# Optimization experiments

Measured on AMD Instinct MI355X. Metric: run time of the kernel, lower is better.

The kernel has to match this reference:

```python
import jax, jax.numpy as jnp
import numpy as np

B, S, E = 2, 2048, 2048
NQ, NKV, HD = 16, 4, 128
WINDOW = 512
ROPE_BASE = 10000.0


def _rope(x):
    # x: [B, H, S, HD], interleaved even/odd rotation
    half = HD // 2
    freqs = 1.0 / (ROPE_BASE ** (2.0 * jnp.arange(half, dtype=jnp.float32) / HD))
    pos = jnp.arange(x.shape[2], dtype=jnp.float32)
    ang = pos[:, None] * freqs[None, :]            # [S, HD/2]
    cos = jnp.cos(ang)[None, None].astype(x.dtype)  # [1,1,S,HD/2]
    sin = jnp.sin(ang)[None, None].astype(x.dtype)
    xe = x[..., 0::2]
    xo = x[..., 1::2]
    re = xe * cos - xo * sin
    ro = xe * sin + xo * cos
    return jnp.stack([re, ro], axis=-1).reshape(x.shape)


def setup_inputs() -> dict:
    key = jax.random.key(0)
    ks = jax.random.split(key, 9)
    s_in = 1.0 / np.sqrt(E)
    s_out = 1.0 / np.sqrt(NQ * HD)
    return {
        "x": jax.random.normal(ks[0], (B, S, E), jnp.float32),
        "Wq": jax.random.normal(ks[1], (E, NQ * HD), jnp.float32) * s_in,
        "bq": jax.random.normal(ks[2], (NQ * HD,), jnp.float32) * 0.01,
        "Wk": jax.random.normal(ks[3], (E, NKV * HD), jnp.float32) * s_in,
        "bk": jax.random.normal(ks[4], (NKV * HD,), jnp.float32) * 0.01,
        "Wv": jax.random.normal(ks[5], (E, NKV * HD), jnp.float32) * s_in,
        "bv": jax.random.normal(ks[6], (NKV * HD,), jnp.float32) * 0.01,
        "Wo": jax.random.normal(ks[7], (NQ * HD, E), jnp.float32) * s_out,
        "bo": jax.random.normal(ks[8], (E,), jnp.float32) * 0.01,
    }


def reference(x, Wq, bq, Wk, bk, Wv, bv, Wo, bo):
    b, s, _ = x.shape
    q = (x @ Wq + bq).reshape(b, s, NQ, HD).transpose(0, 2, 1, 3)   # [B,NQ,S,HD]
    k = (x @ Wk + bk).reshape(b, s, NKV, HD).transpose(0, 2, 1, 3)  # [B,NKV,S,HD]
    v = (x @ Wv + bv).reshape(b, s, NKV, HD).transpose(0, 2, 1, 3)
    q = _rope(q)
    k = _rope(k)
    rep = NQ // NKV
    k = jnp.repeat(k, rep, axis=1)  # [B,NQ,S,HD], matches torch repeat pattern
    v = jnp.repeat(v, rep, axis=1)
    scores = jnp.einsum("bhqd,bhkd->bhqk", q, k) / np.sqrt(HD)
    i = jnp.arange(s)[:, None]
    j = jnp.arange(s)[None, :]
    allowed = (j <= i) & ((i - j) <= WINDOW)  # sliding-window causal mask
    scores = jnp.where(allowed[None, None], scores, -jnp.inf)
    weights = jax.nn.softmax(scores, axis=-1)
    out = jnp.einsum("bhqk,bhkd->bhqd", weights, v)
    out = out.transpose(0, 2, 1, 3).reshape(b, s, NQ * HD)
    return out @ Wo + bo
```

## Files before the change

kernel.cpp:

```cpp
#include <hip/hip_runtime.h>
#include <hip/hip_bf16.h>
#include <math.h>

#define BB 2
#define SS 2048
#define EE 2048
#define NQ 16
#define NKV 4
#define HD 128
#define WINDOW 512

typedef __hip_bfloat16 bf16;
typedef short short8 __attribute__((ext_vector_type(8)));
typedef float f32x4 __attribute__((ext_vector_type(4)));

__device__ __forceinline__ float toF(bf16 v) { return __bfloat162float(v); }
__device__ __forceinline__ bf16 toB(float v) { return __float2bfloat16(v); }

__device__ __forceinline__ void gld_lds16(const void* g, void* l) {
    __builtin_amdgcn_global_load_lds(
        (const __attribute__((address_space(1))) void*)g,
        (__attribute__((address_space(3))) void*)l, 16, 0, 0);
}

__global__ __launch_bounds__(256) void convert_bf16(const float* __restrict__ in,
                                                    bf16* __restrict__ out, int n) {
    int i = (blockIdx.x * 256 + threadIdx.x) * 4;
    if (i >= n) return;
    const float4 v = *(const float4*)(in + i);
    bf16 o[4] = {toB(v.x), toB(v.y), toB(v.z), toB(v.w)};
    *(uint2*)(out + i) = *(const uint2*)o;
}

__global__ __launch_bounds__(256) void convert_transpose(const float* __restrict__ in,
                                                         bf16* __restrict__ out,
                                                         int K, int N) {
    __shared__ float tile[32][33];
    const int t = threadIdx.x;
    const int tx = t & 31, ty = t >> 5;
    const int n0 = blockIdx.x * 32, k0 = blockIdx.y * 32;
#pragma unroll
    for (int r = 0; r < 4; r++) {
        int k = k0 + ty + r * 8;
        tile[ty + r * 8][tx] = in[(size_t)k * N + n0 + tx];
    }
    __syncthreads();
#pragma unroll
    for (int r = 0; r < 4; r++) {
        int n = n0 + ty + r * 8;
        out[(size_t)n * K + k0 + tx] = toB(tile[tx][ty + r * 8]);
    }
}

template <int MODE>
__global__ __launch_bounds__(256) void mfma_gemm(
    const bf16* __restrict__ A, const bf16* __restrict__ BT,
    const float* __restrict__ b0, const float* __restrict__ b1,
    const float* __restrict__ b2,
    float* __restrict__ Yf,
    bf16* __restrict__ Yq, bf16* __restrict__ Yk, bf16* __restrict__ Yv,
    int M, int N, int K) {
    __shared__ bf16 As[128 * 32];
    __shared__ bf16 Bs[128 * 32];

    const int t = threadIdx.x;
    const int lane = t & 63;
    const int w = t >> 6;
    const int wm = w >> 1, wn = w & 1;
    const int m0 = blockIdx.y * 128, n0 = blockIdx.x * 128;

    const int srow = lane >> 2;
    const int scol = (lane & 3) * 8;

    f32x4 acc[4][4];
#pragma unroll
    for (int i = 0; i < 4; i++)
#pragma unroll
        for (int j = 0; j < 4; j++) acc[i][j] = (f32x4)0.f;

    const int lr = lane & 15;
    const int lq = lane >> 4;

    for (int k0 = 0; k0 < K; k0 += 32) {
#pragma unroll
        for (int s = 0; s < 2; s++) {
            const int c = w * 2 + s;
            gld_lds16(A + (size_t)(m0 + c * 16 + srow) * K + k0 + scol, As + c * 512);
            gld_lds16(BT + (size_t)(n0 + c * 16 + srow) * K + k0 + scol, Bs + c * 512);
        }
        __syncthreads();
        short8 af[4], bfv[4];
#pragma unroll
        for (int i = 0; i < 4; i++)
            af[i] = *(const short8*)(As + (wm * 64 + i * 16 + lr) * 32 + lq * 8);
#pragma unroll
        for (int j = 0; j < 4; j++)
            bfv[j] = *(const short8*)(Bs + (wn * 64 + j * 16 + lr) * 32 + lq * 8);
#pragma unroll
        for (int i = 0; i < 4; i++)
#pragma unroll
            for (int j = 0; j < 4; j++)
                acc[i][j] = __builtin_amdgcn_mfma_f32_16x16x32_bf16(af[i], bfv[j],
                                                                    acc[i][j], 0, 0, 0);
        __syncthreads();
    }

    if (MODE == 0) {
#pragma unroll
        for (int j = 0; j < 4; j++) {
            const int col = n0 + wn * 64 + j * 16 + lr;
            const float bj = b0[col];
#pragma unroll
            for (int i = 0; i < 4; i++) {
                const int row = m0 + wm * 64 + i * 16 + lq * 4;
#pragma unroll
                for (int r = 0; r < 4; r++)
                    Yf[(size_t)(row + r) * N + col] = acc[i][j][r] + bj;
            }
        }
    } else {
        bf16* outp; const float* bias; int ldc, c0;
        if (n0 < 2048)      { outp = Yq; bias = b0; ldc = 2048; c0 = n0; }
        else if (n0 < 2560) { outp = Yk; bias = b1; ldc = 512;  c0 = n0 - 2048; }
        else                { outp = Yv; bias = b2; ldc = 512;  c0 = n0 - 2560; }
#pragma unroll
        for (int j = 0; j < 4; j++) {
            const int col = c0 + wn * 64 + j * 16 + lr;
            const float bj = bias[col];
#pragma unroll
            for (int i = 0; i < 4; i++) {
                const int row = m0 + wm * 64 + i * 16 + lq * 4;
#pragma unroll
                for (int r = 0; r < 4; r++)
                    outp[(size_t)(row + r) * ldc + col] = toB(acc[i][j][r] + bj);
            }
        }
    }
}

__global__ void rope_kernel(bf16* __restrict__ buf, int H) {
    int idx = blockIdx.x * blockDim.x + threadIdx.x;
    int total = BB * SS * H * (HD / 2);
    if (idx >= total) return;
    int d2 = idx & 63;
    int hh = idx >> 6;
    int h = hh % H;
    int row = hh / H;
    int s = row % SS;
    float freq = expf(-logf(10000.f) * (float)(2 * d2) / (float)HD);
    float ang = (float)s * freq;
    float c = cosf(ang), sn = sinf(ang);
    size_t base = ((size_t)row * H + h) * HD + 2 * d2;
    float xe = toF(buf[base]);
    float xo = toF(buf[base + 1]);
    buf[base]     = toB(xe * c - xo * sn);
    buf[base + 1] = toB(xe * sn + xo * c);
}

__global__ __launch_bounds__(256) void attn_mfma(const bf16* __restrict__ Q,
                                                 const bf16* __restrict__ K,
                                                 const bf16* __restrict__ V,
                                                 bf16* __restrict__ Oout) {
    __shared__ bf16 Ks[64 * 128];
    __shared__ bf16 Vt[128 * 72];
    __shared__ bf16 Ps[4 * 16 * 72];

    const int t = threadIdx.x;
    const int lane = t & 63;
    const int w = t >> 6;
    const int q0 = blockIdx.x * 64;
    const int h = blockIdx.y;
    const int b = blockIdx.z;
    const int hkv = h >> 2;
    const int lr = lane & 15;
    const int lq = lane >> 4;
    const float scale = 0.08838834764831845f;

    short8 aq[4];
    {
        const int q = q0 + w * 16 + lr;
        const bf16* qp = Q + (((size_t)b * SS + q) * NQ + h) * HD + lq * 8;
#pragma unroll
        for (int ks = 0; ks < 4; ks++) aq[ks] = *(const short8*)(qp + ks * 32);
    }

    f32x4 Oa[8];
#pragma unroll
    for (int nb = 0; nb < 8; nb++) Oa[nb] = (f32x4)0.f;
    float mprev[4] = {-3.0e38f, -3.0e38f, -3.0e38f, -3.0e38f};
    float lsum[4] = {0.f, 0.f, 0.f, 0.f};

    bf16* Pw = Ps + w * 16 * 72;
    const int jstart = (q0 >= WINDOW) ? (q0 - WINDOW) : 0;

    for (int c0 = jstart; c0 <= q0; c0 += 64) {
        __syncthreads();
#pragma unroll
        for (int s = 0; s < 4; s++) {
            const bf16* gk = K +
                (((size_t)b * SS + c0 + w * 16 + s * 4 + (lane >> 4)) * NKV + hkv) * HD +
                (lane & 15) * 8;
            gld_lds16(gk, Ks + (w * 16 + s * 4) * 128);
        }
        {
            const int key = t & 63;
            const int dg = (t >> 6) * 8;
            const bf16* gv = V + (((size_t)b * SS + c0 + key) * NKV + hkv) * HD + dg;
#pragma unroll
            for (int it = 0; it < 4; it++) {
                short8 vv = *(const short8*)(gv + it * 32);
#pragma unroll
                for (int j = 0; j < 8; j++)
                    Vt[(dg + it * 32 + j) * 72 + key] = ((const bf16*)&vv)[j];
            }
        }
        __syncthreads();

        f32x4 sa[4];
#pragma unroll
        for (int nb = 0; nb < 4; nb++) sa[nb] = (f32x4)0.f;
#pragma unroll
        for (int ks = 0; ks < 4; ks++) {
#pragma unroll
            for (int nb = 0; nb < 4; nb++) {
                short8 bk = *(const short8*)(Ks + (nb * 16 + lr) * 128 + ks * 32 + lq * 8);
                sa[nb] = __builtin_amdgcn_mfma_f32_16x16x32_bf16(aq[ks], bk, sa[nb], 0, 0, 0);
            }
        }

        const int rowb = q0 + w * 16 + lq * 4;
        float pr[4][4], alpha[4];
#pragma unroll
        for (int r = 0; r < 4; r++) {
            const int row = rowb + r;
            float sv[4];
            float mx = -3.0e38f;
#pragma unroll
            for (int nb = 0; nb < 4; nb++) {
                const int col = c0 + nb * 16 + lr;
                const bool valid = (col <= row) && (row - col <= WINDOW);
                const float s = valid ? sa[nb][r] * scale : -3.0e38f;
                sv[nb] = s;
                mx = fmaxf(mx, s);
            }
#pragma unroll
            for (int off = 1; off < 16; off <<= 1) mx = fmaxf(mx, __shfl_xor(mx, off, 64));
            const float mn = fmaxf(fmaxf(mprev[r], mx), -1.0e30f);
            alpha[r] = __expf(mprev[r] - mn);
            mprev[r] = mn;
            float rs = 0.f;
#pragma unroll
            for (int nb = 0; nb < 4; nb++) {
                const float p = __expf(sv[nb] - mn);
                pr[r][nb] = p;
                rs += p;
            }
#pragma unroll
            for (int off = 1; off < 16; off <<= 1) rs += __shfl_xor(rs, off, 64);
            lsum[r] = lsum[r] * alpha[r] + rs;
        }

#pragma unroll
        for (int r = 0; r < 4; r++)
#pragma unroll
            for (int nb = 0; nb < 4; nb++)
                Pw[(lq * 4 + r) * 72 + nb * 16 + lr] = toB(pr[r][nb]);

#pragma unroll
        for (int nb = 0; nb < 8; nb++)
#pragma unroll
            for (int r = 0; r < 4; r++) Oa[nb][r] *= alpha[r];
#pragma unroll
        for (int ks = 0; ks < 2; ks++) {
            short8 pa = *(const short8*)(Pw + lr * 72 + ks * 32 + lq * 8);
#pragma unroll
            for (int nb = 0; nb < 8; nb++) {
                short8 bv = *(const short8*)(Vt + (nb * 16 + lr) * 72 + ks * 32 + lq * 8);
                Oa[nb] = __builtin_amdgcn_mfma_f32_16x16x32_bf16(pa, bv, Oa[nb], 0, 0, 0);
            }
        }
    }

    float linv[4];
#pragma unroll
    for (int r = 0; r < 4; r++) linv[r] = 1.f / lsum[r];
    const int rowb = q0 + w * 16 + lq * 4;
#pragma unroll
    for (int nb = 0; nb < 8; nb++)
#pragma unroll
        for (int r = 0; r < 4; r++)
            Oout[(((size_t)b * SS + rowb + r) * NQ + h) * HD + nb * 16 + lr] =
                toB(Oa[nb][r] * linv[r]);
}

extern "C" void kernel_launch(void* const* d_in, const int* in_sizes, int n_in,
                              void* d_out, int out_size, void* d_ws, size_t ws_size,
                              hipStream_t stream) {
    const float* x  = (const float*)d_in[0];
    const float* Wq = (const float*)d_in[1];
    const float* bq = (const float*)d_in[2];
    const float* Wk = (const float*)d_in[3];
    const float* bk = (const float*)d_in[4];
    const float* Wv = (const float*)d_in[5];
    const float* bv = (const float*)d_in[6];
    const float* Wo = (const float*)d_in[7];
    const float* bo = (const float*)d_in[8];
    float* out = (float*)d_out;

    const int M   = BB * SS;
    const int DQ  = NQ * HD;
    const int DKV = NKV * HD;
    const int NPK = DQ + 2 * DKV;

    bf16* xb     = (bf16*)d_ws;
    bf16* WqkvT  = xb + (size_t)M * EE;
    bf16* WoT    = WqkvT + (size_t)NPK * EE;
    bf16* Qb     = WoT + (size_t)EE * DQ;
    bf16* Kb     = Qb + (size_t)M * DQ;
    bf16* Vb     = Kb + (size_t)M * DKV;

    convert_bf16<<<(M * EE / 4 + 255) / 256, 256, 0, stream>>>(x, xb, M * EE);
    convert_transpose<<<dim3(DQ / 32, EE / 32), 256, 0, stream>>>(Wq, WqkvT, EE, DQ);
    convert_transpose<<<dim3(DKV / 32, EE / 32), 256, 0, stream>>>(
        Wk, WqkvT + (size_t)DQ * EE, EE, DKV);
    convert_transpose<<<dim3(DKV / 32, EE / 32), 256, 0, stream>>>(
        Wv, WqkvT + (size_t)(DQ + DKV) * EE, EE, DKV);
    convert_transpose<<<dim3(DQ / 32, DQ / 32), 256, 0, stream>>>(Wo, WoT, DQ, EE);

    mfma_gemm<1><<<dim3(NPK / 128, M / 128), 256, 0, stream>>>(
        xb, WqkvT, bq, bk, bv, nullptr, Qb, Kb, Vb, M, NPK, EE);

    rope_kernel<<<(BB * SS * NQ * (HD / 2) + 255) / 256, 256, 0, stream>>>(Qb, NQ);
    rope_kernel<<<(BB * SS * NKV * (HD / 2) + 255) / 256, 256, 0, stream>>>(Kb, NKV);

    attn_mfma<<<dim3(SS / 64, NQ, BB), 256, 0, stream>>>(Qb, Kb, Vb, Qb);

    mfma_gemm<0><<<dim3(EE / 128, M / 128), 256, 0, stream>>>(
        Qb, WoT, bo, nullptr, nullptr, out, nullptr, nullptr, nullptr, M, EE, DQ);
}
```

Before: 378.2 us.

## Fuse RoPE into QKV GEMM epilogue, swizzle LDS, merge QKV weight transposes

```diff
diff --git a/kernel.cpp b/kernel.cpp
--- a/kernel.cpp
+++ b/kernel.cpp
@@ -40,16 +40,32 @@
     const int tx = t & 31, ty = t >> 5;
     const int n0 = blockIdx.x * 32, k0 = blockIdx.y * 32;
 #pragma unroll
-    for (int r = 0; r < 4; r++) {
-        int k = k0 + ty + r * 8;
-        tile[ty + r * 8][tx] = in[(size_t)k * N + n0 + tx];
-    }
+    for (int r = 0; r < 4; r++)
+        tile[ty + r * 8][tx] = in[(size_t)(k0 + ty + r * 8) * N + n0 + tx];
     __syncthreads();
 #pragma unroll
-    for (int r = 0; r < 4; r++) {
-        int n = n0 + ty + r * 8;
-        out[(size_t)n * K + k0 + tx] = toB(tile[tx][ty + r * 8]);
-    }
+    for (int r = 0; r < 4; r++)
+        out[(size_t)(n0 + ty + r * 8) * K + k0 + tx] = toB(tile[tx][ty + r * 8]);
+}
+
+__global__ __launch_bounds__(256) void convert_transpose_qkv(
+    const float* __restrict__ Wq, const float* __restrict__ Wk,
+    const float* __restrict__ Wv, bf16* __restrict__ out) {
+    __shared__ float tile[32][33];
+    const int t = threadIdx.x;
+    const int tx = t & 31, ty = t >> 5;
+    const int n0 = blockIdx.x * 32, k0 = blockIdx.y * 32;
+    const float* src; int N, nl0;
+    if (n0 < 2048)      { src = Wq; N = 2048; nl0 = n0; }
+    else if (n0 < 2560) { src = Wk; N = 512;  nl0 = n0 - 2048; }
+    else                { src = Wv; N = 512;  nl0 = n0 - 2560; }
+#pragma unroll
+    for (int r = 0; r < 4; r++)
+        tile[ty + r * 8][tx] = src[(size_t)(k0 + ty + r * 8) * N + nl0 + tx];
+    __syncthreads();
+#pragma unroll
+    for (int r = 0; r < 4; r++)
+        out[(size_t)(n0 + ty + r * 8) * 2048 + k0 + tx] = toB(tile[tx][ty + r * 8]);
 }
 
 template <int MODE>
@@ -70,7 +86,8 @@
     const int m0 = blockIdx.y * 128, n0 = blockIdx.x * 128;
 
     const int srow = lane >> 2;
-    const int scol = (lane & 3) * 8;
+    const int sg   = lane & 3;
+    const int scol = (sg ^ ((srow >> 1) & 3)) * 8;
 
     f32x4 acc[4][4];
 #pragma unroll
@@ -80,6 +97,7 @@
 
     const int lr = lane & 15;
     const int lq = lane >> 4;
+    const int slotr = (lq ^ ((lr >> 1) & 3)) * 8;
 
     for (int k0 = 0; k0 < K; k0 += 32) {
 #pragma unroll
@@ -92,10 +110,10 @@
         short8 af[4], bfv[4];
 #pragma unroll
         for (int i = 0; i < 4; i++)
-            af[i] = *(const short8*)(As + (wm * 64 + i * 16 + lr) * 32 + lq * 8);
+            af[i] = *(const short8*)(As + (wm * 64 + i * 16 + lr) * 32 + slotr);
 #pragma unroll
         for (int j = 0; j < 4; j++)
-            bfv[j] = *(const short8*)(Bs + (wn * 64 + j * 16 + lr) * 32 + lq * 8);
+            bfv[j] = *(const short8*)(Bs + (wn * 64 + j * 16 + lr) * 32 + slotr);
 #pragma unroll
         for (int i = 0; i < 4; i++)
 #pragma unroll
@@ -119,42 +137,43 @@
             }
         }
     } else {
-        bf16* outp; const float* bias; int ldc, c0;
-        if (n0 < 2048)      { outp = Yq; bias = b0; ldc = 2048; c0 = n0; }
-        else if (n0 < 2560) { outp = Yk; bias = b1; ldc = 512;  c0 = n0 - 2048; }
-        else                { outp = Yv; bias = b2; ldc = 512;  c0 = n0 - 2560; }
+        bf16* outp; const float* bias; int ldc, c0; bool dorope;
+        if (n0 < 2048)      { outp = Yq; bias = b0; ldc = 2048; c0 = n0;        dorope = true; }
+        else if (n0 < 2560) { outp = Yk; bias = b1; ldc = 512;  c0 = n0 - 2048; dorope = true; }
+        else                { outp = Yv; bias = b2; ldc = 512;  c0 = n0 - 2560; dorope = false; }
 #pragma unroll
         for (int j = 0; j < 4; j++) {
             const int col = c0 + wn * 64 + j * 16 + lr;
             const float bj = bias[col];
-#pragma unroll
-            for (int i = 0; i < 4; i++) {
-                const int row = m0 + wm * 64 + i * 16 + lq * 4;
-#pragma unroll
-                for (int r = 0; r < 4; r++)
-                    outp[(size_t)(row + r) * ldc + col] = toB(acc[i][j][r] + bj);
+            if (dorope) {
+                const int d2 = (col & 127) >> 1;
+                const bool odd = col & 1;
+                const float freq = __expf(-0.14384103622589045f * (float)d2);
+#pragma unroll
+                for (int i = 0; i < 4; i++) {
+                    const int row = m0 + wm * 64 + i * 16 + lq * 4;
+#pragma unroll
+                    for (int r = 0; r < 4; r++) {
+                        const float v = acc[i][j][r] + bj;
+                        const float p = __shfl_xor(v, 1, 64);
+                        const float ang = (float)((row + r) & (SS - 1)) * freq;
+                        float sn, cs;
+                        __sincosf(ang, &sn, &cs);
+                        const float o = odd ? (p * sn + v * cs) : (v * cs - p * sn);
+                        outp[(size_t)(row + r) * ldc + col] = toB(o);
+                    }
+                }
+            } else {
+#pragma unroll
+                for (int i = 0; i < 4; i++) {
+                    const int row = m0 + wm * 64 + i * 16 + lq * 4;
+#pragma unroll
+                    for (int r = 0; r < 4; r++)
+                        outp[(size_t)(row + r) * ldc + col] = toB(acc[i][j][r] + bj);
+                }
             }
         }
     }
-}
-
-__global__ void rope_kernel(bf16* __restrict__ buf, int H) {
-    int idx = blockIdx.x * blockDim.x + threadIdx.x;
-    int total = BB * SS * H * (HD / 2);
-    if (idx >= total) return;
-    int d2 = idx & 63;
-    int hh = idx >> 6;
-    int h = hh % H;
-    int row = hh / H;
-    int s = row % SS;
-    float freq = expf(-logf(10000.f) * (float)(2 * d2) / (float)HD);
-    float ang = (float)s * freq;
-    float c = cosf(ang), sn = sinf(ang);
-    size_t base = ((size_t)row * H + h) * HD + 2 * d2;
-    float xe = toF(buf[base]);
-    float xo = toF(buf[base + 1]);
-    buf[base]     = toB(xe * c - xo * sn);
-    buf[base + 1] = toB(xe * sn + xo * c);
 }
 
 __global__ __launch_bounds__(256) void attn_mfma(const bf16* __restrict__ Q,
@@ -320,19 +339,12 @@
     bf16* Vb     = Kb + (size_t)M * DKV;
 
     convert_bf16<<<(M * EE / 4 + 255) / 256, 256, 0, stream>>>(x, xb, M * EE);
-    convert_transpose<<<dim3(DQ / 32, EE / 32), 256, 0, stream>>>(Wq, WqkvT, EE, DQ);
-    convert_transpose<<<dim3(DKV / 32, EE / 32), 256, 0, stream>>>(
-        Wk, WqkvT + (size_t)DQ * EE, EE, DKV);
-    convert_transpose<<<dim3(DKV / 32, EE / 32), 256, 0, stream>>>(
-        Wv, WqkvT + (size_t)(DQ + DKV) * EE, EE, DKV);
+    convert_transpose_qkv<<<dim3(NPK / 32, EE / 32), 256, 0, stream>>>(Wq, Wk, Wv, WqkvT);
     convert_transpose<<<dim3(DQ / 32, DQ / 32), 256, 0, stream>>>(Wo, WoT, DQ, EE);
 
     mfma_gemm<1><<<dim3(NPK / 128, M / 128), 256, 0, stream>>>(
         xb, WqkvT, bq, bk, bv, nullptr, Qb, Kb, Vb, M, NPK, EE);
 
-    rope_kernel<<<(BB * SS * NQ * (HD / 2) + 255) / 256, 256, 0, stream>>>(Qb, NQ);
-    rope_kernel<<<(BB * SS * NKV * (HD / 2) + 255) / 256, 256, 0, stream>>>(Kb, NKV);
-
     attn_mfma<<<dim3(SS / 64, NQ, BB), 256, 0, stream>>>(Qb, Kb, Vb, Qb);
 
     mfma_gemm<0><<<dim3(EE / 128, M / 128), 256, 0, stream>>>(
```

Measured after the change: 329.4 us. -12.9%, faster.
